# Performance work log

Hardware: AMD Instinct MI355X
Metric: run time of the kernel (lower is better)

Reference implementation:

```python
import jax, jax.numpy as jnp
import numpy as np
import math

B, S, HID, H = 4, 4096, 1024, 16
DH = HID // H  # 64

def setup_inputs() -> dict:
    key = jax.random.key(0)
    ks = jax.random.split(key, 6)
    query = jax.random.normal(ks[0], (B, S, HID), dtype=jnp.float32)
    key_t = jax.random.normal(ks[1], (B, S, HID), dtype=jnp.float32)
    value = jax.random.normal(ks[2], (B, S, HID), dtype=jnp.float32)
    attn_mask = jax.random.normal(ks[3], (B, S, H, H), dtype=jnp.float32)
    # nn.Linear(hidden, 3*hidden): weight (3H, H), bias (3H,)
    W_qkv = jax.random.normal(ks[4], (3 * HID, HID), dtype=jnp.float32) * (1.0 / math.sqrt(HID))
    b_qkv = jax.random.normal(ks[5], (3 * HID,), dtype=jnp.float32) * 0.01
    return {"query": query, "key": key_t, "value": value, "attn_mask": attn_mask,
            "W_qkv": W_qkv, "b_qkv": b_qkv}

def reference(query, key, value, attn_mask, W_qkv, b_qkv):
    # fused QKV projection (only `query` is used, matching the source)
    qkv = jnp.einsum('bsh,oh->bso', query, W_qkv) + b_qkv  # (B,S,3*HID)
    q, k, v = jnp.split(qkv, 3, axis=-1)
    q = q.reshape(B, S, H, DH)
    k = k.reshape(B, S, H, DH)
    v = v.reshape(B, S, H, DH)
    # NOTE: no (B,H,S,D) permute in the source -> scores are head-vs-head per position
    scale = 1.0 / math.sqrt(DH)
    qk = jnp.einsum('bshd,bsgd->bshg', q, k) * scale + attn_mask  # (B,S,H,H)
    attn_weight = jax.nn.softmax(qk, axis=-1)
    # dropout_p=0 (eval): identity
    o = jnp.einsum('bshg,bsgd->bshd', attn_weight, v)  # (B,S,H,DH)
    return o.reshape(B, S, HID)
```

## Files before the change

### kernel.cpp

```cpp
#include <hip/hip_runtime.h>
#include <cstdint>
#include <cstddef>


typedef __attribute__((ext_vector_type(8))) short bf16x8;
typedef __attribute__((ext_vector_type(4))) short bf16x4;
typedef __attribute__((ext_vector_type(4))) float f32x4;

__device__ inline unsigned short f2bf(float f) {
  unsigned int i = __float_as_uint(f);
  i += 0x7fff + ((i >> 16) & 1);
  return (unsigned short)(i >> 16);
}

__device__ inline void async16(const void* g, void* l) {
  __builtin_amdgcn_global_load_lds(
      (const __attribute__((address_space(1))) void*)g,
      (__attribute__((address_space(3))) void*)l, 16, 0, 0);
}

__global__ __launch_bounds__(256) void cast2_kernel(const float* __restrict__ in0,
                                                    unsigned short* __restrict__ out0,
                                                    int n0,
                                                    const float* __restrict__ in1,
                                                    unsigned short* __restrict__ out1,
                                                    int n1) {
  int i = (blockIdx.x * 256 + threadIdx.x) * 4;
  const float* src; unsigned short* dst;
  if (i < n0) { src = in0 + i; dst = out0 + i; }
  else {
    int j = i - n0;
    if (j >= n1) return;
    src = in1 + j; dst = out1 + j;
  }
  float4 v = *(const float4*)src;
  union { unsigned short u[4]; unsigned long long ll; } o;
  o.u[0] = f2bf(v.x); o.u[1] = f2bf(v.y); o.u[2] = f2bf(v.z); o.u[3] = f2bf(v.w);
  *(unsigned long long*)dst = o.ll;
}

#define GK 1024
#define GN 3072
__global__ __launch_bounds__(512, 2) void gemm_qkv(const unsigned short* __restrict__ A,
                                                   const unsigned short* __restrict__ Bm,
                                                   const float* __restrict__ bias,
                                                   unsigned short* __restrict__ C,
                                                   int base) {
  __shared__ unsigned short As[2][256][64];
  __shared__ unsigned short Bs[2][256][64];

  const int bid = base + blockIdx.x;
  const int swz = (bid & 7) * 96 + (bid >> 3);
  const int m0 = (swz / 12) * 256;
  const int n0 = (swz % 12) * 256;

  const int tid  = threadIdx.x;
  const int lane = tid & 63;
  const int wave = tid >> 6;
  const int wm = wave & 1;
  const int wn = wave >> 1;
  const int fr = lane & 15;
  const int fq = lane >> 4;

  const int r0 = tid >> 3;
  const int c0 = (tid & 7) ^ (r0 & 7);
  const unsigned short* gA = A  + (size_t)(m0 + r0) * GK + c0 * 8;
  const unsigned short* gB = Bm + (size_t)(n0 + r0) * GK + c0 * 8;
  const int ls0 = wave * 512;

#define STAGE_A(tt, hh) do {                                                   \
    unsigned short* lb_ = &As[(tt) & 1][(hh) * 128][0];                        \
    const unsigned short* g_ = gA + (size_t)(hh) * 128 * GK + (tt) * 64;       \
    async16(g_, lb_ + ls0);                                                    \
    async16(g_ + (size_t)64 * GK, lb_ + 4096 + ls0);                           \
  } while (0)
#define STAGE_B(tt, hh) do {                                                   \
    unsigned short* lb_ = &Bs[(tt) & 1][(hh) * 128][0];                        \
    const unsigned short* g_ = gB + (size_t)(hh) * 128 * GK + (tt) * 64;       \
    async16(g_, lb_ + ls0);                                                    \
    async16(g_ + (size_t)64 * GK, lb_ + 4096 + ls0);                           \
  } while (0)

  f32x4 acc[8][4] = {};

  STAGE_A(0, 0); STAGE_A(0, 1); STAGE_B(0, 0); STAGE_B(0, 1);
  STAGE_B(1, 0); STAGE_A(1, 0); STAGE_B(1, 1);

  for (int t = 0; t < 16; ++t) {
    const int cur = t & 1;
    if (t == 0)       { asm volatile("s_waitcnt vmcnt(6)" ::: "memory"); }
    else if (t == 15) { asm volatile("s_waitcnt vmcnt(0)" ::: "memory"); }
    else              { asm volatile("s_waitcnt vmcnt(8)" ::: "memory"); }
    __builtin_amdgcn_s_barrier();
    __builtin_amdgcn_sched_barrier(0);

    bf16x8 bfr[4][2];
    #pragma unroll
    for (int p = 0; p < 4; ++p) {
      bf16x8 af[2][2];
      #pragma unroll
      for (int ii = 0; ii < 2; ++ii) {
        const int rA = (p * 2 + ii) * 32 + wm * 16 + fr;
        #pragma unroll
        for (int ks = 0; ks < 2; ++ks)
          af[ii][ks] = *(const bf16x8*)&As[cur][rA][((ks * 4 + fq) ^ (rA & 7)) * 8];
      }
      if (p == 0) {
        #pragma unroll
        for (int j = 0; j < 4; ++j) {
          const int rB = wn * 64 + j * 16 + fr;
          #pragma unroll
          for (int ks = 0; ks < 2; ++ks)
            bfr[j][ks] = *(const bf16x8*)&Bs[cur][rB][((ks * 4 + fq) ^ (rB & 7)) * 8];
        }
        if (t + 1 < 16) { STAGE_A(t + 1, 1); }
      }
      if (p == 1) {
        asm volatile("s_waitcnt vmcnt(8)" ::: "memory");
      }
      if (p == 2 && t + 2 < 16) { STAGE_B(t + 2, 0); }
      if (p == 3 && t + 2 < 16) { STAGE_A(t + 2, 0); STAGE_B(t + 2, 1); }

      __builtin_amdgcn_s_barrier();
      __builtin_amdgcn_sched_barrier(0);
      __builtin_amdgcn_s_setprio(1);
      #pragma unroll
      for (int ks = 0; ks < 2; ++ks)
        #pragma unroll
        for (int ii = 0; ii < 2; ++ii)
          #pragma unroll
          for (int j = 0; j < 4; ++j)
            acc[p * 2 + ii][j] = __builtin_amdgcn_mfma_f32_16x16x32_bf16(
                af[ii][ks], bfr[j][ks], acc[p * 2 + ii][j], 0, 0, 0);
      __builtin_amdgcn_s_setprio(0);
      __builtin_amdgcn_sched_barrier(0);
    }
  }
#undef STAGE_A
#undef STAGE_B

  #pragma unroll
  for (int i = 0; i < 8; ++i) {
    #pragma unroll
    for (int j = 0; j < 4; ++j) {
      const int col = n0 + wn * 64 + j * 16 + fr;
      const float bc = bias[col];
      const int rowb = m0 + i * 32 + wm * 16 + fq * 4;
      #pragma unroll
      for (int rr = 0; rr < 4; ++rr)
        C[(size_t)(rowb + rr) * GN + col] = f2bf(acc[i][j][rr] + bc);
    }
  }
}

__global__ __launch_bounds__(256, 4) void attn_kernel(const unsigned short* __restrict__ QKV,
                                                      const float* __restrict__ mask,
                                                      float* __restrict__ out) {
  __shared__ unsigned short shV[4][1024];
  const int wave = threadIdx.x >> 6;
  const int lane = threadIdx.x & 63;
  const int pos = blockIdx.x * 4 + wave;

  const unsigned short* row = QKV + (size_t)pos * 3072;

  async16(&row[2048 + (size_t)lane * 8], &shV[wave][0]);
  async16(&row[2048 + 512 + (size_t)lane * 8], &shV[wave][512]);

  const int hn  = lane & 15;
  const int grp = lane >> 4;

  const int qk_off = hn * 64 + grp * 8;
  bf16x8 qf0 = *(const bf16x8*)&row[qk_off];
  bf16x8 qf1 = *(const bf16x8*)&row[qk_off + 32];
  bf16x8 kf0 = *(const bf16x8*)&row[1024 + qk_off];
  bf16x8 kf1 = *(const bf16x8*)&row[1024 + qk_off + 32];

  float4 mk = *(const float4*)&mask[(size_t)pos * 256 + hn * 16 + grp * 4];

  f32x4 s = {};
  s = __builtin_amdgcn_mfma_f32_16x16x32_bf16(kf0, qf0, s, 0, 0, 0);
  s = __builtin_amdgcn_mfma_f32_16x16x32_bf16(kf1, qf1, s, 0, 0, 0);

  float sv0 = s[0] * 0.125f + mk.x;
  float sv1 = s[1] * 0.125f + mk.y;
  float sv2 = s[2] * 0.125f + mk.z;
  float sv3 = s[3] * 0.125f + mk.w;
  float mx = fmaxf(fmaxf(sv0, sv1), fmaxf(sv2, sv3));
  mx = fmaxf(mx, __shfl_xor(mx, 16));
  mx = fmaxf(mx, __shfl_xor(mx, 32));
  float p0 = __expf(sv0 - mx), p1 = __expf(sv1 - mx);
  float p2 = __expf(sv2 - mx), p3 = __expf(sv3 - mx);
  float sum = p0 + p1 + p2 + p3;
  sum += __shfl_xor(sum, 16);
  sum += __shfl_xor(sum, 32);
  const float inv = 1.f / sum;

  union { unsigned u[2]; bf16x4 v; } pa;
  pa.u[0] = (unsigned)f2bf(p0 * inv) | ((unsigned)f2bf(p1 * inv) << 16);
  pa.u[1] = (unsigned)f2bf(p2 * inv) | ((unsigned)f2bf(p3 * inv) << 16);

  const int src = grp * 32 + hn;
  unsigned b0 = __shfl((int)pa.u[0], src),      b1 = __shfl((int)pa.u[1], src);
  unsigned b2 = __shfl((int)pa.u[0], src + 16), b3 = __shfl((int)pa.u[1], src + 16);
  if (grp >= 2) { b0 = b1 = b2 = b3 = 0; }
  union { unsigned u[4]; bf16x8 v; } pb;
  pb.u[0] = b0; pb.u[1] = b1; pb.u[2] = b2; pb.u[3] = b3;

  asm volatile("s_waitcnt vmcnt(0)" ::: "memory");

  const unsigned short* va = &shV[wave][(grp & 1) * 8 * 64];
  #pragma unroll
  for (int db = 0; db < 4; ++db) {
    const int e0 = db * 16 + hn;
    union { unsigned u[4]; bf16x8 v; } av;
    #pragma unroll
    for (int jj = 0; jj < 4; ++jj) {
      unsigned lo = va[(2 * jj) * 64 + e0];
      unsigned hi = va[(2 * jj + 1) * 64 + e0];
      av.u[jj] = lo | (hi << 16);
    }
    f32x4 z = {};
    f32x4 o4 = __builtin_amdgcn_mfma_f32_16x16x32_bf16(av.v, pb.v, z, 0, 0, 0);
    *(float4*)(out + (size_t)pos * 1024 + hn * 64 + db * 16 + grp * 4) =
        *(const float4*)&o4;
  }
}

extern "C" void kernel_launch(void* const* d_in, const int* in_sizes, int n_in,
                              void* d_out, int out_size, void* d_ws, size_t ws_size,
                              hipStream_t stream) {
  const float* query = (const float*)d_in[0];
  const float* mask  = (const float*)d_in[3];
  const float* Wqkv  = (const float*)d_in[4];
  const float* bqkv  = (const float*)d_in[5];
  float* out = (float*)d_out;

  unsigned short* qb   = (unsigned short*)d_ws;
  unsigned short* wb   = (unsigned short*)((char*)d_ws + 33554432);
  unsigned short* qkvb = (unsigned short*)((char*)d_ws + 39845888);

  cast2_kernel<<<19456, 256, 0, stream>>>(query, qb, 16777216, Wqkv, wb, 3145728);

  gemm_qkv<<<256, 512, 0, stream>>>(qb, wb, bqkv, qkvb, 0);
  gemm_qkv<<<256, 512, 0, stream>>>(qb, wb, bqkv, qkvb, 256);
  gemm_qkv<<<256, 512, 0, stream>>>(qb, wb, bqkv, qkvb, 512);

  attn_kernel<<<4096, 256, 0, stream>>>(qkvb, mask, out);
}
```

Measured before the change: 320.2 us.

## Load GEMM A fragments directly from global into registers, merge three launches

The QKV GEMM no longer stages the A tile through LDS. Each wave loads its A fragments straight from global memory into registers, double-buffered across MFMA phases, while only B goes through LDS with one barrier per k-step. The three 256-block launches are merged into a single 768-block launch. This halves LDS use and removes most per-phase barriers, but A is now read without sharing across waves, which may raise global/L2 traffic and expose load latency.

```diff
diff --git a/kernel.cpp b/kernel.cpp
--- a/kernel.cpp
+++ b/kernel.cpp
@@ -44,12 +44,10 @@
 __global__ __launch_bounds__(512, 2) void gemm_qkv(const unsigned short* __restrict__ A,
                                                    const unsigned short* __restrict__ Bm,
                                                    const float* __restrict__ bias,
-                                                   unsigned short* __restrict__ C,
-                                                   int base) {
-  __shared__ unsigned short As[2][256][64];
+                                                   unsigned short* __restrict__ C) {
   __shared__ unsigned short Bs[2][256][64];
 
-  const int bid = base + blockIdx.x;
+  const int bid = blockIdx.x;
   const int swz = (bid & 7) * 96 + (bid >> 3);
   const int m0 = (swz / 12) * 256;
   const int n0 = (swz % 12) * 256;
@@ -64,80 +62,77 @@
 
   const int r0 = tid >> 3;
   const int c0 = (tid & 7) ^ (r0 & 7);
-  const unsigned short* gA = A  + (size_t)(m0 + r0) * GK + c0 * 8;
   const unsigned short* gB = Bm + (size_t)(n0 + r0) * GK + c0 * 8;
   const int ls0 = wave * 512;
 
-#define STAGE_A(tt, hh) do {                                                   \
-    unsigned short* lb_ = &As[(tt) & 1][(hh) * 128][0];                        \
-    const unsigned short* g_ = gA + (size_t)(hh) * 128 * GK + (tt) * 64;       \
+#define STAGE_B(tt) do {                                                       \
+    unsigned short* lb_ = &Bs[(tt) & 1][0][0];                                 \
+    const unsigned short* g_ = gB + (tt) * 64;                                 \
     async16(g_, lb_ + ls0);                                                    \
-    async16(g_ + (size_t)64 * GK, lb_ + 4096 + ls0);                           \
+    async16(g_ + (size_t)64 * GK,  lb_ + 4096 + ls0);                          \
+    async16(g_ + (size_t)128 * GK, lb_ + 8192 + ls0);                          \
+    async16(g_ + (size_t)192 * GK, lb_ + 12288 + ls0);                         \
   } while (0)
-#define STAGE_B(tt, hh) do {                                                   \
-    unsigned short* lb_ = &Bs[(tt) & 1][(hh) * 128][0];                        \
-    const unsigned short* g_ = gB + (size_t)(hh) * 128 * GK + (tt) * 64;       \
-    async16(g_, lb_ + ls0);                                                    \
-    async16(g_ + (size_t)64 * GK, lb_ + 4096 + ls0);                           \
+
+  const unsigned short* aBase = A + (size_t)(m0 + wm * 16 + fr) * GK + fq * 8;
+#define LOAD_AF(AF, tt, pp) do {                                               \
+    _Pragma("unroll")                                                          \
+    for (int ii = 0; ii < 2; ++ii)                                             \
+      _Pragma("unroll")                                                        \
+      for (int ks = 0; ks < 2; ++ks)                                           \
+        AF[ii][ks] = *(const bf16x8*)&aBase[(size_t)(((pp) * 2 + ii) * 32) * GK \
+                                            + (tt) * 64 + ks * 32];            \
   } while (0)
 
+#define READ_B8(bp) do {                                                       \
+    _Pragma("unroll")                                                          \
+    for (int j = 0; j < 4; ++j) {                                              \
+      const int rB = wn * 64 + j * 16 + fr;                                    \
+      _Pragma("unroll")                                                        \
+      for (int ks = 0; ks < 2; ++ks)                                           \
+        bfr[j][ks] = *(const bf16x8*)&Bs[bp][rB][((ks * 4 + fq) ^ (rB & 7)) * 8]; \
+    } } while (0)
+
+#define MFMA16(ph, AF) do {                                                    \
+    __builtin_amdgcn_s_setprio(1);                                             \
+    _Pragma("unroll")                                                          \
+    for (int ks = 0; ks < 2; ++ks)                                             \
+      _Pragma("unroll")                                                        \
+      for (int ii = 0; ii < 2; ++ii)                                           \
+        _Pragma("unroll")                                                      \
+        for (int j = 0; j < 4; ++j)                                            \
+          acc[(ph) * 2 + ii][j] = __builtin_amdgcn_mfma_f32_16x16x32_bf16(     \
+              AF[ii][ks], bfr[j][ks], acc[(ph) * 2 + ii][j], 0, 0, 0);         \
+    __builtin_amdgcn_s_setprio(0);                                             \
+  } while (0)
+
   f32x4 acc[8][4] = {};
-
-  STAGE_A(0, 0); STAGE_A(0, 1); STAGE_B(0, 0); STAGE_B(0, 1);
-  STAGE_B(1, 0); STAGE_A(1, 0); STAGE_B(1, 1);
+  bf16x8 afA[2][2], afB[2][2];
+  bf16x8 bfr[4][2];
+
+  STAGE_B(0);
+  LOAD_AF(afA, 0, 0);
 
   for (int t = 0; t < 16; ++t) {
     const int cur = t & 1;
-    if (t == 0)       { asm volatile("s_waitcnt vmcnt(6)" ::: "memory"); }
-    else if (t == 15) { asm volatile("s_waitcnt vmcnt(0)" ::: "memory"); }
-    else              { asm volatile("s_waitcnt vmcnt(8)" ::: "memory"); }
-    __builtin_amdgcn_s_barrier();
+    asm volatile("s_waitcnt vmcnt(4)\n\ts_barrier" ::: "memory");
     __builtin_amdgcn_sched_barrier(0);
 
-    bf16x8 bfr[4][2];
-    #pragma unroll
-    for (int p = 0; p < 4; ++p) {
-      bf16x8 af[2][2];
-      #pragma unroll
-      for (int ii = 0; ii < 2; ++ii) {
-        const int rA = (p * 2 + ii) * 32 + wm * 16 + fr;
-        #pragma unroll
-        for (int ks = 0; ks < 2; ++ks)
-          af[ii][ks] = *(const bf16x8*)&As[cur][rA][((ks * 4 + fq) ^ (rA & 7)) * 8];
-      }
-      if (p == 0) {
-        #pragma unroll
-        for (int j = 0; j < 4; ++j) {
-          const int rB = wn * 64 + j * 16 + fr;
-          #pragma unroll
-          for (int ks = 0; ks < 2; ++ks)
-            bfr[j][ks] = *(const bf16x8*)&Bs[cur][rB][((ks * 4 + fq) ^ (rB & 7)) * 8];
-        }
-        if (t + 1 < 16) { STAGE_A(t + 1, 1); }
-      }
-      if (p == 1) {
-        asm volatile("s_waitcnt vmcnt(8)" ::: "memory");
-      }
-      if (p == 2 && t + 2 < 16) { STAGE_B(t + 2, 0); }
-      if (p == 3 && t + 2 < 16) { STAGE_A(t + 2, 0); STAGE_B(t + 2, 1); }
-
-      __builtin_amdgcn_s_barrier();
-      __builtin_amdgcn_sched_barrier(0);
-      __builtin_amdgcn_s_setprio(1);
-      #pragma unroll
-      for (int ks = 0; ks < 2; ++ks)
-        #pragma unroll
-        for (int ii = 0; ii < 2; ++ii)
-          #pragma unroll
-          for (int j = 0; j < 4; ++j)
-            acc[p * 2 + ii][j] = __builtin_amdgcn_mfma_f32_16x16x32_bf16(
-                af[ii][ks], bfr[j][ks], acc[p * 2 + ii][j], 0, 0, 0);
-      __builtin_amdgcn_s_setprio(0);
-      __builtin_amdgcn_sched_barrier(0);
-    }
-  }
-#undef STAGE_A
+    READ_B8(cur);
+    LOAD_AF(afB, t, 1);
+    MFMA16(0, afA);
+    LOAD_AF(afA, t, 2);
+    MFMA16(1, afB);
+    if (t + 1 < 16) { STAGE_B(t + 1); }
+    LOAD_AF(afB, t, 3);
+    MFMA16(2, afA);
+    if (t + 1 < 16) { LOAD_AF(afA, t + 1, 0); }
+    MFMA16(3, afB);
+  }
 #undef STAGE_B
+#undef LOAD_AF
+#undef READ_B8
+#undef MFMA16
 
   #pragma unroll
   for (int i = 0; i < 8; ++i) {
@@ -241,9 +236,7 @@
 
   cast2_kernel<<<19456, 256, 0, stream>>>(query, qb, 16777216, Wqkv, wb, 3145728);
 
-  gemm_qkv<<<256, 512, 0, stream>>>(qb, wb, bqkv, qkvb, 0);
-  gemm_qkv<<<256, 512, 0, stream>>>(qb, wb, bqkv, qkvb, 256);
-  gemm_qkv<<<256, 512, 0, stream>>>(qb, wb, bqkv, qkvb, 512);
+  gemm_qkv<<<768, 512, 0, stream>>>(qb, wb, bqkv, qkvb);
 
   attn_kernel<<<4096, 256, 0, stream>>>(qkvb, mask, out);
 }
```

After: 421.6 us. 31.7% more time.
